# Kernel optimization log

Hardware: AMD Instinct MI355X
Metric: run time of the kernel (lower is better)

The kernel has to match this reference:

```python
import jax, jax.numpy as jnp
import numpy as np

# 32-entry table: T[j] = 2^(j/32), stored as IEEE-754 fp32 bit patterns (the
# second table_hex assignment in the source, which overrides the first).
TABLE_HEX = [1065353216, 1065536903, 1065724611, 1065916431, 1066112450, 1066312762,
             1066517459, 1066726640, 1066940400, 1067158842, 1067382066, 1067610179,
             1067843287, 1068081499, 1068324927, 1068573686, 1068827891, 1069087663,
             1069353124, 1069624397, 1069901610, 1070184894, 1070474380, 1070770206,
             1071072509, 1071381432, 1071697119, 1072019719, 1072349383, 1072686266,
             1073030525, 1073382323]

def _table_bits():
    # Unpack each 32-bit constant into 32 {0,1} float pulses, MSB first
    # (matches _make_constant: pulse[..., i] = (ival >> (31 - i)) & 1).
    ivals = np.asarray(TABLE_HEX, dtype=np.uint32)
    shifts = np.arange(31, -1, -1, dtype=np.uint32)
    bits = ((ivals[:, None] >> shifts[None, :]) & np.uint32(1)).astype(np.float32)
    return jnp.asarray(bits)  # [32 entries, 32 bit-pulses]

def setup_inputs() -> dict:
    key = jax.random.key(0)
    # 5 select bits per lookup (b4..b0, MSB first), as 0/1 float spikes.
    idx_bits = jax.random.bernoulli(key, 0.5, (1024, 2048, 5)).astype(jnp.float32)
    return {"idx_bits": idx_bits, "table_bits": _table_bits()}

def reference(idx_bits, table_bits):
    # The 31-mux binary select tree with mux(sel, B, A) = A + sel*(B - A) is
    # exactly multilinear interpolation over the 5 select bits. Build the 32
    # multilinear weights w[..., j] = prod_k (b_k if bit k of j else 1-b_k)
    # with j's MSB = b4 (first tree level), then contract with the table.
    w = jnp.ones(idx_bits.shape[:-1] + (1,), dtype=idx_bits.dtype)
    for k in range(5):  # b4 (MSB) first, b0 (LSB) last
        b = idx_bits[..., k:k + 1]
        w = jnp.concatenate([w * (1.0 - b), w * b], axis=-1)
    # w: [..., 32] selection weights; table_bits: [32, 32] bit payloads.
    return jnp.einsum('...j,jp->...p', w, table_bits)
```

## Files before the change

### kernel.cpp

```cpp
#include <hip/hip_runtime.h>


typedef float floatx4 __attribute__((ext_vector_type(4)));

__global__ __launch_bounds__(256) void spike_lookup_kernel(
    const float* __restrict__ idx_bits,
    const float* __restrict__ table_bits,
    float* __restrict__ out,
    long n_pos) {
  const long total4 = n_pos * 8;
  const long nthreads = (long)gridDim.x * blockDim.x;
  const long gid = (long)blockIdx.x * blockDim.x + threadIdx.x;
  const int lane8 = (int)(gid & 7);
  const int bit_lane = lane8 < 5 ? lane8 : 4;
  const unsigned shift = threadIdx.x & 56;

#pragma unroll 4
  for (long g = gid; g < total4; g += nthreads) {
    const long pos = g >> 3;
    const float v = idx_bits[pos * 5 + bit_lane];
    const unsigned long long m = __ballot(v > 0.5f);
    const unsigned j = (unsigned)((m >> shift) & 31ull);

    const floatx4 row = *reinterpret_cast<const floatx4*>(
        table_bits + (j << 5) + (lane8 << 2));

    __builtin_nontemporal_store(row,
                                reinterpret_cast<floatx4*>(out + (g << 2)));
  }
}

extern "C" void kernel_launch(void* const* d_in, const int* in_sizes, int n_in,
                              void* d_out, int out_size, void* d_ws, size_t ws_size,
                              hipStream_t stream) {
  const float* idx_bits = (const float*)d_in[0];
  const float* table_bits = (const float*)d_in[1];
  float* out = (float*)d_out;

  const long n_pos = in_sizes[0] / 5;
  const int block = 256;
  const int grid = 4096;

  spike_lookup_kernel<<<grid, block, 0, stream>>>(idx_bits, table_bits, out,
                                                  n_pos);
}
```

Baseline: 52.20 us.

## Split lookup into index-compute kernel and table-write kernel via workspace byte buffer

The fused kernel is split in two. The first kernel reads the five select bits, forms the 5-bit index with a ballot and writes one byte per position to the workspace. The second kernel reads those bytes and streams the matching table rows to the output with nontemporal stores. The aim is to keep the input reads and the output writes out of the same kernel, at the cost of an extra launch and an extra round trip of the byte buffer through memory. If the workspace is too small, the code falls back to the fused kernel.

```diff
diff --git a/kernel.cpp b/kernel.cpp
--- a/kernel.cpp
+++ b/kernel.cpp
@@ -3,8 +3,29 @@
 
 typedef float floatx4 __attribute__((ext_vector_type(4)));
 
-__global__ __launch_bounds__(256) void spike_lookup_kernel(
+__global__ __launch_bounds__(256) void spike_jidx_kernel(
     const float* __restrict__ idx_bits,
+    unsigned char* __restrict__ jout,
+    long n_pos) {
+  const long total = n_pos * 8;
+  const long nthreads = (long)gridDim.x * blockDim.x;
+  const long gid = (long)blockIdx.x * blockDim.x + threadIdx.x;
+  const int lane8 = (int)(gid & 7);
+  const int bit_lane = lane8 < 5 ? lane8 : 4;
+  const unsigned shift = threadIdx.x & 56;
+
+#pragma unroll 4
+  for (long g = gid; g < total; g += nthreads) {
+    const long pos = g >> 3;
+    const float v = idx_bits[pos * 5 + bit_lane];
+    const unsigned long long m = __ballot(v > 0.5f);
+    const unsigned j = (unsigned)((m >> shift) & 31ull);
+    if (lane8 == 0) jout[pos] = (unsigned char)j;
+  }
+}
+
+__global__ __launch_bounds__(256) void spike_write_kernel(
+    const unsigned char* __restrict__ jin,
     const float* __restrict__ table_bits,
     float* __restrict__ out,
     long n_pos) {
@@ -12,19 +33,35 @@
   const long nthreads = (long)gridDim.x * blockDim.x;
   const long gid = (long)blockIdx.x * blockDim.x + threadIdx.x;
   const int lane8 = (int)(gid & 7);
+
+#pragma unroll 4
+  for (long g = gid; g < total4; g += nthreads) {
+    const long pos = g >> 3;
+    const unsigned j = jin[pos];
+    const floatx4 row = *reinterpret_cast<const floatx4*>(
+        table_bits + (j << 5) + (lane8 << 2));
+    __builtin_nontemporal_store(row,
+                                reinterpret_cast<floatx4*>(out + (g << 2)));
+  }
+}
+
+__global__ __launch_bounds__(256) void spike_lookup_kernel(
+    const float* __restrict__ idx_bits, const float* __restrict__ table_bits,
+    float* __restrict__ out, long n_pos) {
+  const long total4 = n_pos * 8;
+  const long nthreads = (long)gridDim.x * blockDim.x;
+  const long gid = (long)blockIdx.x * blockDim.x + threadIdx.x;
+  const int lane8 = (int)(gid & 7);
   const int bit_lane = lane8 < 5 ? lane8 : 4;
   const unsigned shift = threadIdx.x & 56;
-
 #pragma unroll 4
   for (long g = gid; g < total4; g += nthreads) {
     const long pos = g >> 3;
     const float v = idx_bits[pos * 5 + bit_lane];
     const unsigned long long m = __ballot(v > 0.5f);
     const unsigned j = (unsigned)((m >> shift) & 31ull);
-
     const floatx4 row = *reinterpret_cast<const floatx4*>(
         table_bits + (j << 5) + (lane8 << 2));
-
     __builtin_nontemporal_store(row,
                                 reinterpret_cast<floatx4*>(out + (g << 2)));
   }
@@ -41,6 +78,13 @@
   const int block = 256;
   const int grid = 4096;
 
-  spike_lookup_kernel<<<grid, block, 0, stream>>>(idx_bits, table_bits, out,
-                                                  n_pos);
+  if (ws_size >= (size_t)n_pos) {
+    unsigned char* jbuf = (unsigned char*)d_ws;
+    spike_jidx_kernel<<<grid, block, 0, stream>>>(idx_bits, jbuf, n_pos);
+    spike_write_kernel<<<grid, block, 0, stream>>>(jbuf, table_bits, out,
+                                                   n_pos);
+  } else {
+    spike_lookup_kernel<<<grid, block, 0, stream>>>(idx_bits, table_bits, out,
+                                                    n_pos);
+  }
 }
```

Result: slower. 77.03 us (+47.6%).
